# Optimization experiments

Measured on AMD Instinct MI355X. Metric: run time of the kernel, lower is better.

The kernel has to match this reference:

```python
import jax, jax.numpy as jnp
import numpy as np


def conv2d(x, w, b=None, pad=0):
    # x: [B,C,H,W], w: [O,I,kh,kw]
    out = jax.lax.conv_general_dilated(
        x, w, window_strides=(1, 1), padding=[(pad, pad), (pad, pad)],
        dimension_numbers=('NCHW', 'OIHW', 'NCHW'))
    if b is not None:
        out = out + b[None, :, None, None]
    return out


def setup_inputs() -> dict:
    key = jax.random.key(0)
    ks = jax.random.split(key, 10)
    B, C, W, H, N, G = 8, 256, 64, 64, 1024, 32
    s = jnp.float32(0.02)  # small init so softmax is not saturated
    return {
        'input_graph': jax.random.normal(ks[0], (B, N, G), jnp.float32),
        'input_image': jax.random.normal(ks[1], (B, C, W, H), jnp.float32),
        'Wq': jax.random.normal(ks[2], (C, C), jnp.float32) * s,
        'bq': jnp.zeros((C,), jnp.float32),
        'Wk': jax.random.normal(ks[3], (C, G), jnp.float32) * s,
        'bk': jnp.zeros((C,), jnp.float32),
        'Wv': jax.random.normal(ks[4], (C, G), jnp.float32) * s,
        'bv': jnp.zeros((C,), jnp.float32),
        'conv1_w': jax.random.normal(ks[5], (C, C, 1, 1), jnp.float32) * s,
        'bn_gamma': jnp.ones((C,), jnp.float32),
        'bn_beta': jnp.zeros((C,), jnp.float32),
        'bn_mean': jnp.zeros((C,), jnp.float32),
        'bn_var': jnp.ones((C,), jnp.float32),
        'conv2_w': jax.random.normal(ks[6], (C, C, 3, 3), jnp.float32) * s,
        'conv2_b': jnp.zeros((C,), jnp.float32),
        'conv3_w': jax.random.normal(ks[7], (C, C, 1, 1), jnp.float32) * s,
        'conv3_b': jnp.zeros((C,), jnp.float32),
    }


def reference(input_graph, input_image, Wq, bq, Wk, bk, Wv, bv,
              conv1_w, bn_gamma, bn_beta, bn_mean, bn_var,
              conv2_w, conv2_b, conv3_w, conv3_b):
    B, C, W, H = input_image.shape
    P = W * H
    g = jnp.transpose(input_graph, (0, 2, 1))  # [B,G,N]
    # 1x1 conv1d projections == per-position matmuls
    K = jnp.einsum('og,bgn->bon', Wk, g) + bk[None, :, None]   # [B,C,N]
    V = jnp.einsum('og,bgn->bon', Wv, g) + bv[None, :, None]   # [B,C,N]
    x = input_image.reshape(B, C, P)
    Q = jnp.einsum('oc,bcp->bop', Wq, x) + bq[None, :, None]   # [B,C,P]
    # att[b,p,n] = sum_c Q[b,c,p] * K[b,c,n]  (Q was permuted to [B,P,C] in torch)
    att = jnp.einsum('bcp,bcn->bpn', Q, K) / jnp.sqrt(jnp.float32(C))
    # NOTE: original applies Softmax(dim=1) -> over the P (pixel) axis
    att = jax.nn.softmax(att, axis=1)
    # message = V @ att^T : [B,C,N] x [B,N,P] -> [B,C,P]
    msg = jnp.einsum('bcn,bpn->bcp', V, att).reshape(B, C, W, H)
    # Conv_Bn_Activation: 1x1 conv (no bias) + BN (inference) + LeakyReLU(0.1)
    h = conv2d(msg, conv1_w)
    inv = jax.lax.rsqrt(bn_var + jnp.float32(1e-5))
    h = (h - bn_mean[None, :, None, None]) * (bn_gamma * inv)[None, :, None, None] + bn_beta[None, :, None, None]
    h = jnp.where(h > 0, h, jnp.float32(0.1) * h)
    h = conv2d(h, conv2_w, conv2_b, pad=1)  # 3x3, pad 1
    return input_image + conv2d(h, conv3_w, conv3_b)  # 1x1
```

## Files before the change

kernel.cpp:

```cpp
#include <hip/hip_runtime.h>
#include <hip/hip_bf16.h>

typedef __hip_bfloat16 bf16;
typedef unsigned short u16;
typedef __attribute__((ext_vector_type(8))) short  b8v;
typedef __attribute__((ext_vector_type(8))) unsigned short u16x8;
typedef __attribute__((ext_vector_type(4))) unsigned short u16x4;
typedef __attribute__((ext_vector_type(4))) float f32x4;

static __device__ __forceinline__ float us2f(u16 s) {
    unsigned int u = ((unsigned int)s) << 16;
    return __builtin_bit_cast(float, u);
}
static __device__ __forceinline__ u16 f2us(float x) {
    union { bf16 h; u16 s; } v; v.h = __float2bfloat16(x); return v.s;
}
static __device__ __forceinline__ float b2f(bf16 x) { return __bfloat162float(x); }
static __device__ __forceinline__ bf16 f2b(float x) { return __float2bfloat16(x); }
static __device__ __forceinline__ float toF(float x) { return x; }
static __device__ __forceinline__ float toF(bf16 x)  { return b2f(x); }
static __device__ __forceinline__ void stor(float* p, float v) { *p = v; }
static __device__ __forceinline__ void stor(bf16* p,  float v) { *p = f2b(v); }

static __device__ __forceinline__ void gload16(const u16* g, u16* l) {
    __builtin_amdgcn_global_load_lds(
        (const __attribute__((address_space(1))) unsigned int*)g,
        (__attribute__((address_space(3))) unsigned int*)l,
        16, 0, 0);
}


__global__ __launch_bounds__(256) void cast_f2b4(const float* __restrict__ src,
                                                 u16* __restrict__ dst, int n4)
{
    int i = blockIdx.x * 256 + threadIdx.x;
    if (i < n4) {
        float4 v = ((const float4*)src)[i];
        u16x4 o = { f2us(v.x), f2us(v.y), f2us(v.z), f2us(v.w) };
        ((u16x4*)dst)[i] = o;
    }
}

__global__ __launch_bounds__(256) void repack_w2(const float* __restrict__ src,
                                                 u16* __restrict__ dst)
{
    int idx = blockIdx.x * 256 + threadIdx.x;
    int o = idx / 2304, k = idx - o * 2304;
    int tap = k >> 8, c = k & 255;
    dst[idx] = f2us(src[(o * 256 + c) * 9 + tap]);
}

__global__ __launch_bounds__(256) void transpose_cast_x(const float* __restrict__ x,
                                                        u16* __restrict__ xT, int C, int P)
{
    __shared__ u16 t[64][72];
    const int b = blockIdx.z, c0 = blockIdx.y * 64, p0 = blockIdx.x * 64;
    const int tid = threadIdx.x;
    const int r = tid >> 2, q = tid & 3;
    const float* src = x + ((size_t)b * C + c0 + r) * P + p0 + q * 16;
#pragma unroll
    for (int i = 0; i < 16; i++) t[q * 16 + i][r] = f2us(src[i]);
    __syncthreads();
    u16* dst = xT + ((size_t)b * P + p0 + r) * C + c0 + q * 16;
    *(u16x8*)dst       = *(u16x8*)&t[r][q * 16];
    *(u16x8*)(dst + 8) = *(u16x8*)&t[r][q * 16 + 8];
}

template<int EPI, typename TA, typename TB, typename TC>
__global__ __launch_bounds__(256) void gemm_any(
    const TA* __restrict__ A, const TB* __restrict__ B, TC* __restrict__ C,
    int M, int Nn, int Kd,
    long saM, long saK, long aB,
    long sbK, long sbN, long bB,
    long scM, long scN, long cB,
    float scale, const float* __restrict__ bias)
{
    __shared__ float As[16][65];
    __shared__ float Bs[16][65];
    const int b  = blockIdx.z;
    const TA* Ab = A + (long)b * aB;
    const TB* Bb = B + (long)b * bB;
    const int m0 = blockIdx.y * 64, n0 = blockIdx.x * 64;
    const int tid = threadIdx.x;
    const int tx = tid & 15, ty = tid >> 4;
    const bool kfA = (saK == 1);
    const bool nfB = (sbN == 1);
    float acc[4][4] = {};

    for (int k0 = 0; k0 < Kd; k0 += 16) {
#pragma unroll
        for (int i = 0; i < 4; i++) {
            int idx = tid + i * 256; int mm, kk;
            if (kfA) { kk = idx & 15; mm = idx >> 4; }
            else     { mm = idx & 63; kk = idx >> 6; }
            As[kk][mm] = toF(Ab[(long)(m0 + mm) * saM + (long)(k0 + kk) * saK]);
        }
#pragma unroll
        for (int i = 0; i < 4; i++) {
            int idx = tid + i * 256; int nn, kk;
            if (nfB) { nn = idx & 63; kk = idx >> 6; }
            else     { kk = idx & 15; nn = idx >> 4; }
            Bs[kk][nn] = toF(Bb[(long)(k0 + kk) * sbK + (long)(n0 + nn) * sbN]);
        }
        __syncthreads();
#pragma unroll
        for (int kk = 0; kk < 16; kk++) {
            float a[4], bb[4];
#pragma unroll
            for (int i = 0; i < 4; i++) a[i]  = As[kk][ty * 4 + i];
#pragma unroll
            for (int j = 0; j < 4; j++) bb[j] = Bs[kk][tx * 4 + j];
#pragma unroll
            for (int i = 0; i < 4; i++)
#pragma unroll
                for (int j = 0; j < 4; j++) acc[i][j] += a[i] * bb[j];
        }
        __syncthreads();
    }
#pragma unroll
    for (int i = 0; i < 4; i++) {
        int m = m0 + ty * 4 + i;
        float add0 = (EPI == 0 && bias) ? bias[m] : 0.f;
#pragma unroll
        for (int j = 0; j < 4; j++) {
            int n = n0 + tx * 4 + j;
            float v = acc[i][j] * scale + add0;
            if (EPI == 3 && bias) v += bias[n];
            stor(&C[(long)b * cB + (long)m * scM + (long)n * scN], v);
        }
    }
}

template<int EPI, bool CT, typename TC, int NTILE>
__global__ __launch_bounds__(256) void gemm_mfma(
    const u16* __restrict__ A, const u16* __restrict__ Bt, TC* __restrict__ Cc,
    int M, int N, int K, int lda, int ldb, int ldc,
    long aBat, long bBat, long cBat,
    float scale, const float* __restrict__ bias,
    const float* __restrict__ gamma, const float* __restrict__ beta,
    const float* __restrict__ mean,  const float* __restrict__ var,
    const float* __restrict__ resid, long rBat, int ldr,
    float* __restrict__ csum)
{
    constexpr int NI = NTILE / 32;
    __shared__ u16 Al[128 * 32];
    __shared__ u16 Bl[NTILE * 32];
    __shared__ float red[(EPI == 3) ? 256 : 1];
    __shared__ u16 tbuf[(EPI == 3) ? 64 * 136 : 1];
    const int bat = blockIdx.z;
    const int m0 = blockIdx.y * 128, n0 = blockIdx.x * NTILE;
    const int tid = threadIdx.x;
    const int lane = tid & 63, wid = tid >> 6;
    const int wr = wid >> 1, wc = wid & 1;
    const int fr = lane & 15, fq = lane >> 4;
    const int sc = ((lane & 3) ^ ((lane >> 3) & 3)) * 8;
    const int axs = (fq ^ ((fr >> 1) & 3)) * 8;

    const u16* gA = A  + (size_t)bat * aBat + (size_t)(m0 + wid * 32 + (lane >> 2)) * lda + sc;
    const u16* gB = Bt + (size_t)bat * bBat + (size_t)(n0 + wid * (NTILE / 4) + (lane >> 2)) * ldb + sc;
    u16* lA = &Al[(wid * 32) * 32];
    u16* lB = &Bl[(wid * (NTILE / 4)) * 32];
    const size_t a16 = (size_t)16 * lda, b16 = (size_t)16 * ldb;

    f32x4 acc[4][NI];
#pragma unroll
    for (int i = 0; i < 4; i++)
#pragma unroll
        for (int j = 0; j < NI; j++) acc[i][j] = (f32x4){0.f, 0.f, 0.f, 0.f};

    for (int k0 = 0; k0 < K; k0 += 32) {
        gload16(gA + k0,       lA);
        gload16(gA + k0 + a16, lA + 16 * 32);
        gload16(gB + k0,       lB);
        if constexpr (NTILE == 128) gload16(gB + k0 + b16, lB + 16 * 32);
        __syncthreads();
        b8v a[4], b[NI];
#pragma unroll
        for (int mi = 0; mi < 4; mi++) a[mi] = *(const b8v*)&Al[(wr * 64 + mi * 16 + fr) * 32 + axs];
#pragma unroll
        for (int ni = 0; ni < NI; ni++) b[ni] = *(const b8v*)&Bl[(wc * (NTILE / 2) + ni * 16 + fr) * 32 + axs];
#pragma unroll
        for (int mi = 0; mi < 4; mi++)
#pragma unroll
            for (int ni = 0; ni < NI; ni++)
                acc[mi][ni] = __builtin_amdgcn_mfma_f32_16x16x32_bf16(a[mi], b[ni], acc[mi][ni], 0, 0, 0);
        __syncthreads();
    }

    const int mbase = m0 + wr * 64, nbase = n0 + wc * (NTILE / 2);

    if constexpr (EPI == 3) {
        float cs[NI];
#pragma unroll
        for (int ni = 0; ni < NI; ni++) cs[ni] = 0.f;
#pragma unroll
        for (int h = 0; h < 2; h++) {
#pragma unroll
            for (int mh = 0; mh < 2; mh++) {
                const int mi = h * 2 + mh;
                const int trow = wr * 32 + mh * 16 + fq * 4;
#pragma unroll
                for (int ni = 0; ni < NI; ni++) {
                    const int n = nbase + ni * 16 + fr;
                    const float tqv = bias ? bias[(size_t)bat * N + n] : 0.f;
                    f32x4 v = acc[mi][ni];
#pragma unroll
                    for (int j = 0; j < 4; j++) {
                        float x = __expf((v[j] + tqv) * scale);
                        cs[ni] += x;
                        tbuf[(trow + j) * 136 + wc * 64 + ni * 16 + fr] = f2us(x);
                    }
                }
            }
            __syncthreads();
#pragma unroll
            for (int it = 0; it < 4; it++) {
                const int idx = it * 256 + tid;
                const int row = idx >> 4, ng = idx & 15;
                const int m = m0 + (row >> 5) * 64 + h * 32 + (row & 31);
                u16x8 v8 = *(const u16x8*)&tbuf[row * 136 + ng * 8];
                *(u16x8*)((u16*)Cc + (size_t)bat * cBat + (size_t)m * ldc + n0 + ng * 8) = v8;
            }
            __syncthreads();
        }
#pragma unroll
        for (int ni = 0; ni < NI; ni++) {
            float s = cs[ni];
            s += __shfl_xor(s, 16, 64);
            s += __shfl_xor(s, 32, 64);
            if (fq == 0) red[wr * 128 + wc * 64 + ni * 16 + fr] = s;
        }
        __syncthreads();
        if (tid < NTILE) {
            float s = red[tid] + red[128 + tid];
            csum[((size_t)bat * gridDim.y + blockIdx.y) * ldc + n0 + tid] = s;
        }
        return;
    }

#pragma unroll
    for (int mi = 0; mi < 4; mi++) {
        float esc[4], ead[4];
#pragma unroll
        for (int j = 0; j < 4; j++) {
            int m = mbase + mi * 16 + fq * 4 + j;
            if (EPI == 1) {
                float sc2 = gamma[m] * rsqrtf(var[m] + 1e-5f);
                esc[j] = sc2; ead[j] = beta[m] - mean[m] * sc2;
            } else {
                esc[j] = scale;
                ead[j] = ((EPI == 0 || EPI == 2) && bias) ? bias[m] : 0.f;
            }
        }
#pragma unroll
        for (int ni = 0; ni < NI; ni++) {
            f32x4 v = acc[mi][ni];
            const int n = nbase + ni * 16 + fr;
            if (CT) {
                const int mb = mbase + mi * 16 + fq * 4;
                if constexpr (EPI == 4) {
                    const float bb = bias ? bias[n] : 0.f;
                    float4 rv = *(const float4*)&resid[(size_t)bat * rBat + (size_t)n * ldr + mb];
                    float4 o4;
                    o4.x = v[0] * scale + bb + rv.x;
                    o4.y = v[1] * scale + bb + rv.y;
                    o4.z = v[2] * scale + bb + rv.z;
                    o4.w = v[3] * scale + bb + rv.w;
                    *(float4*)((float*)Cc + (size_t)bat * cBat + (size_t)n * ldc + mb) = o4;
                } else {
                    const long crow = (EPI == 1)
                        ? (long)(((n >> 6) + 1) * 66 + (n & 63) + 1)
                        : (long)n;
                    u16x4 pk;
#pragma unroll
                    for (int j = 0; j < 4; j++) {
                        float x = v[j] * esc[j] + ead[j];
                        if (EPI == 1) x = x > 0.f ? x : 0.1f * x;
                        pk[j] = f2us(x);
                    }
                    *(u16x4*)((u16*)Cc + (size_t)bat * cBat + (size_t)crow * ldc + mb) = pk;
                }
            } else {
#pragma unroll
                for (int j = 0; j < 4; j++) {
                    int m = mbase + mi * 16 + fq * 4 + j;
                    float x = v[j] * esc[j] + ead[j];
                    if (EPI == 1) x = x > 0.f ? x : 0.1f * x;
                    if (EPI == 2) x += resid[(size_t)bat * rBat + (size_t)m * ldr + n];
                    TC* p = Cc + (size_t)bat * cBat + (size_t)m * ldc + n;
                    if constexpr (sizeof(TC) == 2) *(u16*)p = f2us(x); else *(float*)p = x;
                }
            }
        }
    }
}

__global__ __launch_bounds__(256) void conv3x3_mfma(
    const u16* __restrict__ Wt, const u16* __restrict__ Xp, u16* __restrict__ Y,
    const float* __restrict__ bias)
{
    const int C = 256, P = 4096, K = 2304;
    __shared__ u16 Al[2][128 * 32];
    __shared__ u16 Bl[64 * 64];
    const int bat = blockIdx.z;
    const int m0 = blockIdx.y * 128;
    const int y0 = blockIdx.x;
    const int tid = threadIdx.x;
    const int lane = tid & 63, wid = tid >> 6;
    const int wr = wid >> 1, wc = wid & 1;
    const int fr = lane & 15, fq = lane >> 4;
    const int scA = ((lane & 3) ^ ((lane >> 3) & 3)) * 8;
    const int axs = (fq ^ ((fr >> 1) & 3)) * 8;

    const u16* Ag = Wt + (size_t)(m0 + wid * 32 + (lane >> 2)) * K + scA;
    u16* lA0 = &Al[0][(wid * 32) * 32];
    u16* lA1 = &Al[1][(wid * 32) * 32];
    const u16* Xb = Xp + (size_t)bat * 66 * 66 * 256;

    const int brow = (lane >> 3), bq = lane & 7;

    f32x4 acc[4][2];
#pragma unroll
    for (int i = 0; i < 4; i++)
#pragma unroll
        for (int j = 0; j < 2; j++) acc[i][j] = (f32x4){0.f, 0.f, 0.f, 0.f};

    for (int k0 = 0; k0 < K; k0 += 64) {
        const int tap = k0 >> 8, c0k = k0 & 255;
        const int dy = tap / 3 - 1, dxv = tap - (tap / 3) * 3 - 1;
        const int syp = y0 + dy + 1;
        gload16(Ag + k0,                       lA0);
        gload16(Ag + k0 + (size_t)16 * K,      lA0 + 16 * 32);
        gload16(Ag + k0 + 32,                  lA1);
        gload16(Ag + k0 + 32 + (size_t)16 * K, lA1 + 16 * 32);
#pragma unroll
        for (int h = 0; h < 2; h++) {
            const int g = wid * 2 + h;
            const int r = g * 8 + brow;
            const int qs = bq ^ (r & 7);
            const u16* src = Xb + ((size_t)syp * 66 + (r + dxv + 1)) * 256 + c0k + qs * 8;
            gload16(src, &Bl[g * 512]);
        }
        __syncthreads();
#pragma unroll
        for (int t = 0; t < 2; t++) {
            b8v a[4], b[2];
#pragma unroll
            for (int mi = 0; mi < 4; mi++) a[mi] = *(const b8v*)&Al[t][(wr * 64 + mi * 16 + fr) * 32 + axs];
#pragma unroll
            for (int ni = 0; ni < 2; ni++) {
                const int row = wc * 32 + ni * 16 + fr;
                const int ch = ((t * 4 + fq) ^ (fr & 7)) * 8;
                b[ni] = *(const b8v*)&Bl[row * 64 + ch];
            }
#pragma unroll
            for (int mi = 0; mi < 4; mi++)
#pragma unroll
                for (int ni = 0; ni < 2; ni++)
                    acc[mi][ni] = __builtin_amdgcn_mfma_f32_16x16x32_bf16(a[mi], b[ni], acc[mi][ni], 0, 0, 0);
        }
        __syncthreads();
    }

    const int mbase = m0 + wr * 64, nbase = y0 * 64 + wc * 32;
#pragma unroll
    for (int mi = 0; mi < 4; mi++) {
        const int mb = mbase + mi * 16 + fq * 4;
        float bb[4];
#pragma unroll
        for (int j = 0; j < 4; j++) bb[j] = bias[mb + j];
#pragma unroll
        for (int ni = 0; ni < 2; ni++) {
            const int n = nbase + ni * 16 + fr;
            u16x4 pk;
#pragma unroll
            for (int j = 0; j < 4; j++) pk[j] = f2us(acc[mi][ni][j] + bb[j]);
            *(u16x4*)&Y[(size_t)bat * P * C + (size_t)n * C + mb] = pk;
        }
    }
}


__global__ __launch_bounds__(256) void tq_dot(const u16* __restrict__ Kt,
                                              const float* __restrict__ bq,
                                              float* __restrict__ tq, int N, int C)
{
    const int n = blockIdx.x * 256 + threadIdx.x, b = blockIdx.y;
    const u16* row = Kt + ((size_t)b * N + n) * C;
    float s = 0.f;
    for (int c = 0; c < C; c += 8) {
        u16x8 v = *(const u16x8*)&row[c];
#pragma unroll
        for (int j = 0; j < 8; j++) s += us2f(v[j]) * bq[c + j];
    }
    tq[(size_t)b * N + n] = s;
}

__global__ __launch_bounds__(256) void colsum_merge(const float* __restrict__ part,
                                                    float* __restrict__ sinv, int N, int PC)
{
    const int n = blockIdx.x * 256 + threadIdx.x, b = blockIdx.y;
    const float* pc = part + (size_t)b * PC * N + n;
    float s = 0.f;
    for (int c = 0; c < PC; c++) s += pc[(size_t)c * N];
    sinv[(size_t)b * N + n] = 1.f / s;
}

__global__ __launch_bounds__(256) void scale_vt(u16* __restrict__ Vt,
                                                const float* __restrict__ sinv,
                                                int N, int C)
{
    const size_t base = ((size_t)blockIdx.x * 256 + threadIdx.x) * 8;
    const int n = (int)((base / C) % N);
    const int b = (int)(base / ((size_t)N * C));
    const float s = sinv[(size_t)b * N + n];
    u16x8 v = *(u16x8*)&Vt[base];
#pragma unroll
    for (int j = 0; j < 8; j++) v[j] = f2us(us2f(v[j]) * s);
    *(u16x8*)&Vt[base] = v;
}

__global__ __launch_bounds__(256) void zero_halo(u16* __restrict__ Xp)
{
    int i = blockIdx.x * 256 + threadIdx.x;
    const int ch8 = i & 31; i >>= 5;
    const int hp = i % 260;
    const int b = i / 260;
    int py, px;
    if (hp < 66)       { py = 0;  px = hp; }
    else if (hp < 132) { py = 65; px = hp - 66; }
    else if (hp < 196) { py = hp - 132 + 1; px = 0; }
    else               { py = hp - 196 + 1; px = 65; }
    u16x8 z = {0, 0, 0, 0, 0, 0, 0, 0};
    *(u16x8*)&Xp[(((size_t)b * 66 + py) * 66 + px) * 256 + ch8 * 8] = z;
}


extern "C" void kernel_launch(void* const* d_in, const int* in_sizes, int n_in,
                              void* d_out, int out_size, void* d_ws, size_t ws_size,
                              hipStream_t stream)
{
    const float* graph = (const float*)d_in[0];
    const float* image = (const float*)d_in[1];
    const float* Wq  = (const float*)d_in[2];
    const float* bq  = (const float*)d_in[3];
    const float* Wk  = (const float*)d_in[4];
    const float* bk  = (const float*)d_in[5];
    const float* Wv  = (const float*)d_in[6];
    const float* bv  = (const float*)d_in[7];
    const float* c1w = (const float*)d_in[8];
    const float* gam = (const float*)d_in[9];
    const float* bet = (const float*)d_in[10];
    const float* mea = (const float*)d_in[11];
    const float* var = (const float*)d_in[12];
    const float* c2w = (const float*)d_in[13];
    const float* c2b = (const float*)d_in[14];
    const float* c3w = (const float*)d_in[15];
    const float* c3b = (const float*)d_in[16];
    float* out = (float*)d_out;

    const int B = 8, C = 256, P = 4096, N = 1024, G = 32;
    const size_t MiB = 1024 * 1024, KiB = 1024;
    char* ws = (char*)d_ws;
    char* dob = (char*)d_out;
    u16* WqT  = (u16*)(ws);
    u16* E    = (u16*)(ws);
    u16* xT   = (u16*)(ws + 64 * MiB);
    u16* Kt   = (u16*)(ws + 80 * MiB);
    u16* VV   = (u16*)(ws + 80 * MiB);
    u16* Vt   = (u16*)(ws + 84 * MiB);
    u16* h2T  = (u16*)(ws);
    u16* c2w_b = (u16*)(ws + 17 * MiB);
    u16* c3w_b = (u16*)(ws + 19 * MiB);
    float* part = (float*)(dob);
    u16* KWt   = (u16*)(dob + 2 * MiB);
    float* tqb = (float*)(dob + 6 * MiB);
    float* sinv = (float*)(dob + 7 * MiB);
    u16* c1w_b = (u16*)(dob + 8 * MiB);
    u16* h1p   = (u16*)(dob + 14 * MiB);

    transpose_cast_x<<<dim3(P / 64, C / 64, B), 256, 0, stream>>>(image, xT, C, P);
    transpose_cast_x<<<dim3(4, 4, 1), 256, 0, stream>>>(Wq, WqT, 256, 256);
    cast_f2b4<<<64, 256, 0, stream>>>(c1w, c1w_b, 16384);
    gemm_any<3, float, float, bf16><<<dim3(C / 64, N / 64, B), 256, 0, stream>>>(
        graph, Wk, (bf16*)Kt, N, C, G,
        G, 1, (long)N * G,   1, G, 0,   C, 1, (long)N * C, 1.f, bk);
    gemm_any<3, float, float, bf16><<<dim3(C / 64, N / 64, B), 256, 0, stream>>>(
        graph, Wv, (bf16*)Vt, N, C, G,
        G, 1, (long)N * G,   1, G, 0,   C, 1, (long)N * C, 1.f, bv);
    gemm_mfma<0, false, u16, 64><<<dim3(C / 64, N / 128, B), 256, 0, stream>>>(
        Kt, WqT, KWt, N, C, C, C, C, C,
        (long)N * C, 0, (long)N * C, 1.f, nullptr,
        nullptr, nullptr, nullptr, nullptr, nullptr, 0, 0, nullptr);
    tq_dot<<<dim3(N / 256, B), 256, 0, stream>>>(Kt, bq, tqb, N, C);
    gemm_mfma<3, false, u16, 128><<<dim3(N / 128, P / 128, B), 256, 0, stream>>>(
        xT, KWt, E, P, N, C, C, C, N,
        (long)P * C, (long)N * C, (long)P * N, 0.0625f, tqb,
        nullptr, nullptr, nullptr, nullptr, nullptr, 0, 0, part);
    colsum_merge<<<dim3(N / 256, B), 256, 0, stream>>>(part, sinv, N, P / 128);
    scale_vt<<<dim3((int)((size_t)B * N * C / 8 / 256)), 256, 0, stream>>>(Vt, sinv, N, C);
    gemm_mfma<0, false, u16, 64><<<dim3(N / 64, C / 128, B), 256, 0, stream>>>(
        c1w_b, Vt, VV, C, N, C, C, C, N,
        0, (long)N * C, (long)C * N, 1.f, nullptr,
        nullptr, nullptr, nullptr, nullptr, nullptr, 0, 0, nullptr);
    gemm_mfma<1, true, u16, 64><<<dim3(P / 64, C / 128, B), 256, 0, stream>>>(
        VV, E, h1p, C, P, N, N, N, C,
        (long)C * N, (long)P * N, (long)66 * 66 * C, 1.f, nullptr,
        gam, bet, mea, var, nullptr, 0, 0, nullptr);
    zero_halo<<<260, 256, 0, stream>>>(h1p);
    repack_w2<<<2304, 256, 0, stream>>>(c2w, c2w_b);
    cast_f2b4<<<64, 256, 0, stream>>>(c3w, c3w_b, 16384);
    conv3x3_mfma<<<dim3(P / 64, C / 128, B), 256, 0, stream>>>(c2w_b, h1p, h2T, c2b);
    gemm_mfma<4, true, float, 64><<<dim3(C / 64, P / 128, B), 256, 0, stream>>>(
        h2T, c3w_b, out, P, C, C, C, C, P,
        (long)P * C, 0, (long)C * P, 1.f, c3b,
        nullptr, nullptr, nullptr, nullptr, image, (long)C * P, P, nullptr);
}
```

Baseline: 229.9 us.

## Enlarge conv3x3 and conv1 GEMM N-tiles to 128 and swizzle block order

The 3x3 conv kernel now computes a 128-pixel tile (two image rows) per block instead of 64, giving each wave a 64x64 output sub-tile with 16 accumulators. This doubles reuse of the weight tile loaded per k-step. The conv1/BN GEMM also moves to a 128-wide N tile. All gemm_mfma and conv blocks now remap their block index with an interleaved swizzle so neighbouring blocks are spread across groups of eight, aiming for better cache locality. The cost is more registers and LDS per block and half as many blocks, which can lower occupancy.

```diff
diff --git a/kernel.cpp b/kernel.cpp
--- a/kernel.cpp
+++ b/kernel.cpp
@@ -148,7 +148,11 @@
     __shared__ float red[(EPI == 3) ? 256 : 1];
     __shared__ u16 tbuf[(EPI == 3) ? 64 * 136 : 1];
     const int bat = blockIdx.z;
-    const int m0 = blockIdx.y * 128, n0 = blockIdx.x * NTILE;
+    const int nxy = gridDim.x * gridDim.y;
+    const int fid = blockIdx.y * gridDim.x + blockIdx.x;
+    const int swzid = (fid & 7) * (nxy >> 3) + (fid >> 3);
+    const int bidx = swzid % gridDim.x, bidy = swzid / gridDim.x;
+    const int m0 = bidy * 128, n0 = bidx * NTILE;
     const int tid = threadIdx.x;
     const int lane = tid & 63, wid = tid >> 6;
     const int wr = wid >> 1, wc = wid & 1;
@@ -233,7 +237,7 @@
         __syncthreads();
         if (tid < NTILE) {
             float s = red[tid] + red[128 + tid];
-            csum[((size_t)bat * gridDim.y + blockIdx.y) * ldc + n0 + tid] = s;
+            csum[((size_t)bat * gridDim.y + bidy) * ldc + n0 + tid] = s;
         }
         return;
     }
@@ -301,10 +305,15 @@
 {
     const int C = 256, P = 4096, K = 2304;
     __shared__ u16 Al[2][128 * 32];
-    __shared__ u16 Bl[64 * 64];
+    __shared__ u16 Bl[128 * 64];
     const int bat = blockIdx.z;
-    const int m0 = blockIdx.y * 128;
-    const int y0 = blockIdx.x;
+    const int nxy = gridDim.x * gridDim.y;
+    const int fid = blockIdx.y * gridDim.x + blockIdx.x;
+    const int swzid = (fid & 7) * (nxy >> 3) + (fid >> 3);
+    const int bidx = swzid % gridDim.x, bidy = swzid / gridDim.x;
+    const int m0 = bidy * 128;
+    const int p0 = bidx * 128;
+    const int iy0 = bidx * 2;
     const int tid = threadIdx.x;
     const int lane = tid & 63, wid = tid >> 6;
     const int wr = wid >> 1, wc = wid & 1;
@@ -317,52 +326,53 @@
     u16* lA1 = &Al[1][(wid * 32) * 32];
     const u16* Xb = Xp + (size_t)bat * 66 * 66 * 256;
 
-    const int brow = (lane >> 3), bq = lane & 7;
-
-    f32x4 acc[4][2];
+    const int bpx = (lane >> 3), bq = lane & 7;
+
+    f32x4 acc[4][4];
 #pragma unroll
     for (int i = 0; i < 4; i++)
 #pragma unroll
-        for (int j = 0; j < 2; j++) acc[i][j] = (f32x4){0.f, 0.f, 0.f, 0.f};
+        for (int j = 0; j < 4; j++) acc[i][j] = (f32x4){0.f, 0.f, 0.f, 0.f};
 
     for (int k0 = 0; k0 < K; k0 += 64) {
         const int tap = k0 >> 8, c0k = k0 & 255;
         const int dy = tap / 3 - 1, dxv = tap - (tap / 3) * 3 - 1;
-        const int syp = y0 + dy + 1;
         gload16(Ag + k0,                       lA0);
         gload16(Ag + k0 + (size_t)16 * K,      lA0 + 16 * 32);
         gload16(Ag + k0 + 32,                  lA1);
         gload16(Ag + k0 + 32 + (size_t)16 * K, lA1 + 16 * 32);
 #pragma unroll
-        for (int h = 0; h < 2; h++) {
-            const int g = wid * 2 + h;
-            const int r = g * 8 + brow;
-            const int qs = bq ^ (r & 7);
-            const u16* src = Xb + ((size_t)syp * 66 + (r + dxv + 1)) * 256 + c0k + qs * 8;
+        for (int h = 0; h < 4; h++) {
+            const int g = wid * 4 + h;
+            const int px = g * 8 + bpx;
+            const int syp = iy0 + (px >> 6) + dy + 1;
+            const int sxp = (px & 63) + dxv + 1;
+            const int qs = bq ^ (px & 7);
+            const u16* src = Xb + ((size_t)syp * 66 + sxp) * 256 + c0k + qs * 8;
             gload16(src, &Bl[g * 512]);
         }
         __syncthreads();
 #pragma unroll
         for (int t = 0; t < 2; t++) {
-            b8v a[4], b[2];
+            b8v a[4], b[4];
 #pragma unroll
             for (int mi = 0; mi < 4; mi++) a[mi] = *(const b8v*)&Al[t][(wr * 64 + mi * 16 + fr) * 32 + axs];
 #pragma unroll
-            for (int ni = 0; ni < 2; ni++) {
-                const int row = wc * 32 + ni * 16 + fr;
-                const int ch = ((t * 4 + fq) ^ (fr & 7)) * 8;
+            for (int ni = 0; ni < 4; ni++) {
+                const int row = wc * 64 + ni * 16 + fr;
+                const int ch = ((t * 4 + fq) ^ (row & 7)) * 8;
                 b[ni] = *(const b8v*)&Bl[row * 64 + ch];
             }
 #pragma unroll
             for (int mi = 0; mi < 4; mi++)
 #pragma unroll
-                for (int ni = 0; ni < 2; ni++)
+                for (int ni = 0; ni < 4; ni++)
                     acc[mi][ni] = __builtin_amdgcn_mfma_f32_16x16x32_bf16(a[mi], b[ni], acc[mi][ni], 0, 0, 0);
         }
         __syncthreads();
     }
 
-    const int mbase = m0 + wr * 64, nbase = y0 * 64 + wc * 32;
+    const int mbase = m0 + wr * 64, nbase = p0 + wc * 64;
 #pragma unroll
     for (int mi = 0; mi < 4; mi++) {
         const int mb = mbase + mi * 16 + fq * 4;
@@ -370,7 +380,7 @@
 #pragma unroll
         for (int j = 0; j < 4; j++) bb[j] = bias[mb + j];
 #pragma unroll
-        for (int ni = 0; ni < 2; ni++) {
+        for (int ni = 0; ni < 4; ni++) {
             const int n = nbase + ni * 16 + fr;
             u16x4 pk;
 #pragma unroll
@@ -503,14 +513,14 @@
         c1w_b, Vt, VV, C, N, C, C, C, N,
         0, (long)N * C, (long)C * N, 1.f, nullptr,
         nullptr, nullptr, nullptr, nullptr, nullptr, 0, 0, nullptr);
-    gemm_mfma<1, true, u16, 64><<<dim3(P / 64, C / 128, B), 256, 0, stream>>>(
+    gemm_mfma<1, true, u16, 128><<<dim3(P / 128, C / 128, B), 256, 0, stream>>>(
         VV, E, h1p, C, P, N, N, N, C,
         (long)C * N, (long)P * N, (long)66 * 66 * C, 1.f, nullptr,
         gam, bet, mea, var, nullptr, 0, 0, nullptr);
     zero_halo<<<260, 256, 0, stream>>>(h1p);
     repack_w2<<<2304, 256, 0, stream>>>(c2w, c2w_b);
     cast_f2b4<<<64, 256, 0, stream>>>(c3w, c3w_b, 16384);
-    conv3x3_mfma<<<dim3(P / 64, C / 128, B), 256, 0, stream>>>(c2w_b, h1p, h2T, c2b);
+    conv3x3_mfma<<<dim3(P / 128, C / 128, B), 256, 0, stream>>>(c2w_b, h1p, h2T, c2b);
     gemm_mfma<4, true, float, 64><<<dim3(C / 64, P / 128, B), 256, 0, stream>>>(
         h2T, c3w_b, out, P, C, C, C, C, P,
         (long)P * C, 0, (long)C * P, 1.f, c3b,
```

Measured after the change: 222.1 us. 1.04x faster.

## Double K-step per barrier in MFMA GEMM, swizzle block order, widen msg tile

Applied to the files above, without the earlier changes.

The generic MFMA GEMM now loads two 32-wide K slices per iteration into a two-stage LDS buffer, so it runs one pair of barriers per 64 K instead of per 32 K. The epilogue transpose buffer now reuses that LDS. Block IDs are remapped with a stride-8 swizzle to improve L2 locality across neighbouring workgroups. The attention-message GEMM (EPI 1) switches to a 128-wide N tile, and the conv3x3 B-operand swizzle index changes from fr to row (the same value mod 8). The wider tile raises LDS and register use and halves the number of blocks for that GEMM. The swizzle assumes the flattened grid size is divisible by 8.

```diff
diff --git a/kernel.cpp b/kernel.cpp
--- a/kernel.cpp
+++ b/kernel.cpp
@@ -143,12 +143,16 @@
     float* __restrict__ csum)
 {
     constexpr int NI = NTILE / 32;
-    __shared__ u16 Al[128 * 32];
-    __shared__ u16 Bl[NTILE * 32];
+    constexpr int AW = 128 * 32;
+    constexpr int BW = NTILE * 32;
+    __shared__ u16 lds[2][AW + BW];
     __shared__ float red[(EPI == 3) ? 256 : 1];
-    __shared__ u16 tbuf[(EPI == 3) ? 64 * 136 : 1];
     const int bat = blockIdx.z;
-    const int m0 = blockIdx.y * 128, n0 = blockIdx.x * NTILE;
+    const int nxy = gridDim.x * gridDim.y;
+    const int fid = blockIdx.y * gridDim.x + blockIdx.x;
+    const int swzid = (fid & 7) * (nxy >> 3) + (fid >> 3);
+    const int bidx = swzid % gridDim.x, bidy = swzid / gridDim.x;
+    const int m0 = bidy * 128, n0 = bidx * NTILE;
     const int tid = threadIdx.x;
     const int lane = tid & 63, wid = tid >> 6;
     const int wr = wid >> 1, wc = wid & 1;
@@ -158,8 +162,8 @@
 
     const u16* gA = A  + (size_t)bat * aBat + (size_t)(m0 + wid * 32 + (lane >> 2)) * lda + sc;
     const u16* gB = Bt + (size_t)bat * bBat + (size_t)(n0 + wid * (NTILE / 4) + (lane >> 2)) * ldb + sc;
-    u16* lA = &Al[(wid * 32) * 32];
-    u16* lB = &Bl[(wid * (NTILE / 4)) * 32];
+    const int aoff = (wid * 32) * 32;
+    const int boff = AW + (wid * (NTILE / 4)) * 32;
     const size_t a16 = (size_t)16 * lda, b16 = (size_t)16 * ldb;
 
     f32x4 acc[4][NI];
@@ -168,28 +172,38 @@
 #pragma unroll
         for (int j = 0; j < NI; j++) acc[i][j] = (f32x4){0.f, 0.f, 0.f, 0.f};
 
-    for (int k0 = 0; k0 < K; k0 += 32) {
-        gload16(gA + k0,       lA);
-        gload16(gA + k0 + a16, lA + 16 * 32);
-        gload16(gB + k0,       lB);
-        if constexpr (NTILE == 128) gload16(gB + k0 + b16, lB + 16 * 32);
-        __syncthreads();
-        b8v a[4], b[NI];
-#pragma unroll
-        for (int mi = 0; mi < 4; mi++) a[mi] = *(const b8v*)&Al[(wr * 64 + mi * 16 + fr) * 32 + axs];
-#pragma unroll
-        for (int ni = 0; ni < NI; ni++) b[ni] = *(const b8v*)&Bl[(wc * (NTILE / 2) + ni * 16 + fr) * 32 + axs];
-#pragma unroll
-        for (int mi = 0; mi < 4; mi++)
+    for (int k0 = 0; k0 < K; k0 += 64) {
+        gload16(gA + k0,            &lds[0][aoff]);
+        gload16(gA + k0 + a16,      &lds[0][aoff + 16 * 32]);
+        gload16(gA + k0 + 32,       &lds[1][aoff]);
+        gload16(gA + k0 + 32 + a16, &lds[1][aoff + 16 * 32]);
+        gload16(gB + k0,            &lds[0][boff]);
+        if constexpr (NTILE == 128) gload16(gB + k0 + b16, &lds[0][boff + 16 * 32]);
+        gload16(gB + k0 + 32,       &lds[1][boff]);
+        if constexpr (NTILE == 128) gload16(gB + k0 + 32 + b16, &lds[1][boff + 16 * 32]);
+        __syncthreads();
+#pragma unroll
+        for (int t = 0; t < 2; t++) {
+            b8v a[4], b[NI];
+#pragma unroll
+            for (int mi = 0; mi < 4; mi++)
+                a[mi] = *(const b8v*)&lds[t][(wr * 64 + mi * 16 + fr) * 32 + axs];
 #pragma unroll
             for (int ni = 0; ni < NI; ni++)
-                acc[mi][ni] = __builtin_amdgcn_mfma_f32_16x16x32_bf16(a[mi], b[ni], acc[mi][ni], 0, 0, 0);
+                b[ni] = *(const b8v*)&lds[t][AW + (wc * (NTILE / 2) + ni * 16 + fr) * 32 + axs];
+#pragma unroll
+            for (int mi = 0; mi < 4; mi++)
+#pragma unroll
+                for (int ni = 0; ni < NI; ni++)
+                    acc[mi][ni] = __builtin_amdgcn_mfma_f32_16x16x32_bf16(a[mi], b[ni], acc[mi][ni], 0, 0, 0);
+        }
         __syncthreads();
     }
 
     const int mbase = m0 + wr * 64, nbase = n0 + wc * (NTILE / 2);
 
     if constexpr (EPI == 3) {
+        u16* tbuf = &lds[0][0];
         float cs[NI];
 #pragma unroll
         for (int ni = 0; ni < NI; ni++) cs[ni] = 0.f;
@@ -233,7 +247,7 @@
         __syncthreads();
         if (tid < NTILE) {
             float s = red[tid] + red[128 + tid];
-            csum[((size_t)bat * gridDim.y + blockIdx.y) * ldc + n0 + tid] = s;
+            csum[((size_t)bat * gridDim.y + bidy) * ldc + n0 + tid] = s;
         }
         return;
     }
@@ -350,7 +364,7 @@
 #pragma unroll
             for (int ni = 0; ni < 2; ni++) {
                 const int row = wc * 32 + ni * 16 + fr;
-                const int ch = ((t * 4 + fq) ^ (fr & 7)) * 8;
+                const int ch = ((t * 4 + fq) ^ (row & 7)) * 8;
                 b[ni] = *(const b8v*)&Bl[row * 64 + ch];
             }
 #pragma unroll
@@ -503,7 +517,7 @@
         c1w_b, Vt, VV, C, N, C, C, C, N,
         0, (long)N * C, (long)C * N, 1.f, nullptr,
         nullptr, nullptr, nullptr, nullptr, nullptr, 0, 0, nullptr);
-    gemm_mfma<1, true, u16, 64><<<dim3(P / 64, C / 128, B), 256, 0, stream>>>(
+    gemm_mfma<1, true, u16, 128><<<dim3(P / 128, C / 128, B), 256, 0, stream>>>(
         VV, E, h1p, C, P, N, N, N, C,
         (long)C * N, (long)P * N, (long)66 * 66 * C, 1.f, nullptr,
         gam, bet, mea, var, nullptr, 0, 0, nullptr);
```

New measurement: 211.5 us. 1.09x faster.
